# Kernel tuning notes

Hardware: AMD Instinct MI355X
Metric: run time of the kernel (lower is better)

The kernel has to match this reference:

```python
import jax, jax.numpy as jnp
import numpy as np

B, S, M = 1, 1024, 1024          # batch, seq, hidden
H, D, KV = 16, 64, 8             # q heads, head dim, kv heads (kv hardcoded=8)
G = H // KV                      # gqa groups
FF = 3072                        # expert/shared mlp inner dim (hardcoded)
E, K = 64, 8                     # experts, topk (hardcoded)
CAP = 2 * K * S * B // E         # static expert capacity (>= dynamic max -> no drops)
RMS_EPS = 1e-6
F32_EPS = 1.1920929e-07          # torch.finfo(float32).eps


def _rms(x, w, eps=RMS_EPS):
    v = jnp.mean(x * x, axis=-1, keepdims=True)
    return w * (x * jax.lax.rsqrt(v + eps))


def _rotate_half(x):
    d = x.shape[-1] // 2
    return jnp.concatenate([-x[..., d:], x[..., :d]], axis=-1)


def _mlp(x, gu_w, dn_w):
    gu = x @ gu_w                       # [..., 2*FF]
    x1, x2 = gu[..., :FF], gu[..., FF:]
    return (x1 * jax.nn.silu(x2)) @ dn_w


def _topkgating(logits):
    # logits: [T, E] fp32
    gates = jax.nn.softmax(logits, axis=1)
    topv, topi = jax.lax.top_k(gates, K)                 # [T, K]
    gates_s = jnp.clip(jnp.sum(topv, axis=1, keepdims=True), F32_EPS)
    router_probs = gates / gates_s                        # [T, E]
    # priority: cumsum of one-hot over flattened (K, T) order, matching torch
    idx_flat = topi.T.reshape(-1)                         # [K*T]
    mask = jax.nn.one_hot(idx_flat, E, dtype=jnp.int32)   # [K*T, E]
    prio = jnp.cumsum(mask, axis=0) * mask - 1            # [K*T, E]
    prio = prio.reshape(K, -1, E).transpose(1, 0, 2).max(axis=1)  # [T, E]
    valid = (prio >= 0) & (prio < CAP)
    prio = jnp.where(valid, prio, 0)
    dispatch = jax.nn.one_hot(prio, CAP, dtype=jnp.float32) * valid[..., None]  # [T,E,C]
    combine = router_probs[..., None] * dispatch                                 # [T,E,C]
    return combine, dispatch


def setup_inputs() -> dict:
    key = jax.random.key(0)
    ks = jax.random.split(key, 10)
    sc = 0.02
    inv_freq = 1.0 / (10000.0 ** (jnp.arange(0, D, 2, dtype=jnp.float32) / D))
    t = jnp.arange(S, dtype=jnp.float32)
    freqs = jnp.outer(t, inv_freq)                        # [S, D/2]
    emb = jnp.concatenate([freqs, freqs], axis=-1)        # [S, D]
    cos = jnp.broadcast_to(jnp.cos(emb), (B, S, D))
    sin = jnp.broadcast_to(jnp.sin(emb), (B, S, D))
    return {
        'hidden_states': jax.random.normal(ks[0], (B, S, M), jnp.float32),
        'cos': cos,
        'sin': sin,
        'ln1_w': jnp.ones((M,), jnp.float32),
        'ln2_w': jnp.ones((M,), jnp.float32),
        'qkv_w': jax.random.normal(ks[1], (M, (H + 2 * KV) * D), jnp.float32) * sc,
        'o_w': jax.random.normal(ks[2], (H * D, M), jnp.float32) * sc,
        'qn_w': jnp.ones((D,), jnp.float32),
        'kn_w': jnp.ones((D,), jnp.float32),
        'shared_gu_w': jax.random.normal(ks[3], (M, 2 * FF), jnp.float32) * sc,
        'shared_dn_w': jax.random.normal(ks[4], (FF, M), jnp.float32) * sc,
        'gate_w': jax.random.normal(ks[5], (M, E), jnp.float32) * sc,
        'expert_gu_w': jax.random.normal(ks[6], (E, M, 2 * FF), jnp.float32) * sc,
        'expert_dn_w': jax.random.normal(ks[7], (E, FF, M), jnp.float32) * sc,
    }


def reference(hidden_states, cos, sin, ln1_w, ln2_w, qkv_w, o_w, qn_w, kn_w,
              shared_gu_w, shared_dn_w, gate_w, expert_gu_w, expert_dn_w):
    # ---- attention block ----
    hn = _rms(hidden_states, ln1_w)                       # input layernorm
    qkv = (hn @ qkv_w).reshape(B, S, KV, G + 2, D)
    q = qkv[..., :G, :].reshape(B, S, H, D).transpose(0, 2, 1, 3)   # [B,H,S,D]
    k = qkv[..., G, :].transpose(0, 2, 1, 3)                        # [B,KV,S,D]
    v = qkv[..., G + 1, :].transpose(0, 2, 1, 3)                    # [B,KV,S,D]
    c, s_ = cos[:, None], sin[:, None]                    # [B,1,S,D]
    q = q * c + _rotate_half(q) * s_
    k = k * c + _rotate_half(k) * s_
    q = _rms(q, qn_w)
    k = _rms(k, kn_w)
    k = jnp.repeat(k, G, axis=1)                          # GQA expand -> [B,H,S,D]
    v = jnp.repeat(v, G, axis=1)
    scores = jnp.einsum('bhqd,bhkd->bhqk', q, k) / np.sqrt(D)
    causal = jnp.tril(jnp.ones((S, S), bool))
    scores = jnp.where(causal, scores, -1e9)
    attn = jax.nn.softmax(scores, axis=-1)
    ao = jnp.einsum('bhqk,bhkd->bhqd', attn, v).transpose(0, 2, 1, 3).reshape(B, S, H * D)
    h = hidden_states + ao @ o_w                          # residual

    # ---- MoE block ----
    h2 = _rms(h, ln2_w)                                   # post-attn layernorm
    shared = _mlp(h2, shared_gu_w, shared_dn_w)           # [B,S,M]
    x = h2.reshape(-1, M)                                 # [T,M]
    logits = x @ gate_w                                   # fp32 gate
    combine, dispatch = _topkgating(logits)               # [T,E,C]
    dispatched = jnp.einsum('sec,sm->ecm', dispatch, x)   # [E,C,M]
    gu = jnp.einsum('ecm,emf->ecf', dispatched, expert_gu_w)  # [E,C,2*FF]
    x1, x2 = gu[..., :FF], gu[..., FF:]
    eo = jnp.einsum('ecf,efm->ecm', x1 * jax.nn.silu(x2), expert_dn_w)  # [E,C,M]
    combined = jnp.einsum('sec,ecm->sm', combine, eo).reshape(B, S, M)
    return h + shared + combined
```

## Files before the change

kernel.cpp:

```cpp
#include <hip/hip_runtime.h>

#define S 1024
#define MDIM 1024
#define NH 16
#define HD 64
#define NKV 8
#define FF 3072
#define NE 64
#define TOPK 8
#define CAP 256

typedef unsigned short u16;
typedef __attribute__((ext_vector_type(8))) short bf16x8;
typedef __attribute__((ext_vector_type(4))) float f32x4;

__device__ __forceinline__ u16 f2bf(float f) {
    union { float f; unsigned u; } x; x.f = f;
    unsigned r = x.u + 0x7FFFu + ((x.u >> 16) & 1u);
    return (u16)(r >> 16);
}
__device__ __forceinline__ float bf2f(u16 b) {
    union { unsigned u; float f; } x; x.u = ((unsigned)b) << 16;
    return x.f;
}
__device__ __forceinline__ void split1(float x, u16& h, u16& l) {
    h = f2bf(x);
    l = f2bf(x - bf2f(h));
}
__device__ __forceinline__ int swzcol(int row, int G) { return 8 * (G ^ ((row >> 3) & 3)); }

__device__ __forceinline__ void gl_lds16(const u16* g, u16* l) {
    __builtin_amdgcn_global_load_lds(
        (const __attribute__((address_space(1))) unsigned int*)g,
        (__attribute__((address_space(3))) unsigned int*)l, 16, 0, 0);
}

__global__ __launch_bounds__(256) void k_rms1(const float* __restrict__ x,
                                              const float* __restrict__ w,
                                              u16* __restrict__ ohi,
                                              u16* __restrict__ olo) {
    int s = blockIdx.x;
    const float* row = x + (size_t)s * MDIM;
    float v[4]; float ss = 0.f;
#pragma unroll
    for (int i = 0; i < 4; ++i) { v[i] = row[threadIdx.x + i * 256]; ss += v[i] * v[i]; }
#pragma unroll
    for (int of = 32; of; of >>= 1) ss += __shfl_xor(ss, of);
    __shared__ float red[4];
    int wid = threadIdx.x >> 6;
    if ((threadIdx.x & 63) == 0) red[wid] = ss;
    __syncthreads();
    float tot = red[0] + red[1] + red[2] + red[3];
    float sc = rsqrtf(tot * (1.f / MDIM) + 1e-6f);
#pragma unroll
    for (int i = 0; i < 4; ++i) {
        int c = threadIdx.x + i * 256;
        float ov = v[i] * sc * w[c];
        u16 hh, ll; split1(ov, hh, ll);
        ohi[(size_t)s * MDIM + c] = hh;
        olo[(size_t)s * MDIM + c] = ll;
    }
}

template <int EPI>
__global__ __launch_bounds__(256) void k_gemm_split(
    const u16* __restrict__ Ahi, const u16* __restrict__ Alo, int lda,
    const float* __restrict__ B, int ldb,
    float* __restrict__ C, int ldc,
    const float* __restrict__ resid, int M, int K) {
    int m0 = blockIdx.y * 64;
    int n0 = blockIdx.x * 64;
    __shared__ u16 Ah[2][64][32];
    __shared__ u16 Al[2][64][32];
    __shared__ u16 Bh[2][64][40];
    __shared__ u16 Bl[2][64][40];
    int tid = threadIdx.x, lane = tid & 63, wid = tid >> 6;
    int wm = (wid >> 1) * 32, wn = (wid & 1) * 32;
    f32x4 acc[2][2] = {};

    int rt = wid * 16 + (lane >> 2);
    int gsrc = (lane & 3) ^ ((lane >> 4) & 3);
    const u16* ahb = Ahi + (size_t)(m0 + rt) * lda + gsrc * 8;
    const u16* alb = Alo + (size_t)(m0 + rt) * lda + gsrc * 8;

    int nB = tid & 63, kbB = tid >> 6;
    int colB = swzcol(nB, kbB);
    float rb[8];
    auto loadB = [&](int k0) {
        const float* bp = B + (size_t)(k0 + kbB * 8) * ldb + n0 + nB;
#pragma unroll
        for (int i = 0; i < 8; ++i) rb[i] = bp[(size_t)i * ldb];
    };
    auto stageA = [&](int b, int k0) {
        gl_lds16(ahb + k0, &Ah[b][wid * 16][0]);
        gl_lds16(alb + k0, &Al[b][wid * 16][0]);
    };
    auto writeB = [&](int b) {
        bf16x8 hh, ll;
#pragma unroll
        for (int i = 0; i < 8; ++i) { u16 h, l; split1(rb[i], h, l); hh[i] = (short)h; ll[i] = (short)l; }
        *(bf16x8*)&Bh[b][nB][colB] = hh;
        *(bf16x8*)&Bl[b][nB][colB] = ll;
    };

    loadB(0); stageA(0, 0); writeB(0);
    __syncthreads();
    int NT = K / 32;
    for (int t = 0; t < NT; ++t) {
        int c = t & 1;
        if (t + 1 < NT) { loadB((t + 1) * 32); stageA(1 - c, (t + 1) * 32); }
        bf16x8 ah[2], al[2], bh[2], bl[2];
#pragma unroll
        for (int mi = 0; mi < 2; ++mi) {
            int r = wm + mi * 16 + (lane & 15);
            int cA = 8 * ((lane >> 4) ^ ((r >> 2) & 3));
            ah[mi] = *(const bf16x8*)&Ah[c][r][cA];
            al[mi] = *(const bf16x8*)&Al[c][r][cA];
        }
#pragma unroll
        for (int ni = 0; ni < 2; ++ni) {
            int r = wn + ni * 16 + (lane & 15);
            int cc = swzcol(r, lane >> 4);
            bh[ni] = *(const bf16x8*)&Bh[c][r][cc];
            bl[ni] = *(const bf16x8*)&Bl[c][r][cc];
        }
#pragma unroll
        for (int mi = 0; mi < 2; ++mi)
#pragma unroll
            for (int ni = 0; ni < 2; ++ni) {
                acc[mi][ni] = __builtin_amdgcn_mfma_f32_16x16x32_bf16(ah[mi], bh[ni], acc[mi][ni], 0, 0, 0);
                acc[mi][ni] = __builtin_amdgcn_mfma_f32_16x16x32_bf16(ah[mi], bl[ni], acc[mi][ni], 0, 0, 0);
                acc[mi][ni] = __builtin_amdgcn_mfma_f32_16x16x32_bf16(al[mi], bh[ni], acc[mi][ni], 0, 0, 0);
            }
        if (t + 1 < NT) { writeB(1 - c); __syncthreads(); }
    }
#pragma unroll
    for (int mi = 0; mi < 2; ++mi)
#pragma unroll
        for (int ni = 0; ni < 2; ++ni)
#pragma unroll
            for (int r = 0; r < 4; ++r) {
                int row = m0 + wm + mi * 16 + (lane >> 4) * 4 + r;
                int col = n0 + wn + ni * 16 + (lane & 15);
                float v = acc[mi][ni][r];
                if constexpr (EPI == 1) v += resid[(size_t)row * ldc + col];
                C[(size_t)row * ldc + col] = v;
            }
}

template <int TM, int TN, bool SWIGLU>
__global__ __launch_bounds__(256) void k_gemm_bf(
    const u16* __restrict__ A, int lda, long sAe,
    const float* __restrict__ B, long sBe, int ldb,
    u16* __restrict__ C, int ldc, long sCe,
    int K, int pairOff,
    const int* __restrict__ counts, const int* __restrict__ rowidx,
    const u16* __restrict__ Ash, const float* __restrict__ Bsh,
    u16* __restrict__ Csh, int Msh) {
    int z = blockIdx.z;
    int tid = threadIdx.x, lane = tid & 63, wid = tid >> 6;
    int M, m0;
    const int* ridx = nullptr;
    if (z >= NE) {
        int mslot = (z - NE) * 2 + blockIdx.y;
        m0 = mslot * TM;
        M = Msh;
        A = Ash; B = Bsh; C = Csh;
        if (m0 >= M) return;
    } else {
        M = counts[z];
        m0 = blockIdx.y * TM;
        if (m0 >= M) return;
        A += (size_t)z * sAe;
        B += (size_t)z * sBe;
        C += (size_t)z * sCe;
        if (rowidx) ridx = rowidx + z * CAP;
    }
    int n0 = blockIdx.x * TN;

    __shared__ u16 As[2][TM][32];
    __shared__ u16 Bs[2][TN][40];
    __shared__ u16 B2s[2][SWIGLU ? TN : 1][40];

    constexpr int MF = TM / 32;
    constexpr int NI = TN / 32;
    int wm = (wid >> 1) * (TM / 2), wn = (wid & 1) * (TN / 2);

    f32x4 acc[MF][NI] = {};
    f32x4 acc2[SWIGLU ? MF : 1][NI] = {};

    constexpr int NCH = TM / 16;
    constexpr int CPW = (NCH + 3) / 4;
    int arow_in = lane >> 2;
    int gsrc = (lane & 3) ^ ((lane >> 4) & 3);
    const u16* abase[CPW];
#pragma unroll
    for (int i = 0; i < CPW; ++i) {
        int ch = wid + i * 4;
        const u16* p = A;
        if (ch < NCH) {
            int rti = ch * 16 + arow_in;
            int gm = m0 + rti;
            long grow = (gm < M) ? (ridx ? (long)ridx[gm] : (long)gm) : 0;
            p = A + grow * (size_t)lda + gsrc * 8;
        }
        abase[i] = p;
    }
    auto stageA = [&](int b, int k0) {
#pragma unroll
        for (int i = 0; i < CPW; ++i) {
            int ch = wid + i * 4;
            if (ch < NCH) gl_lds16(abase[i] + k0, &As[b][ch * 16][0]);
        }
    };

    constexpr int NKG = 256 / TN;
    constexpr int OPT = 4 / NKG;
    int nB = tid % TN, kgB = tid / TN;
    float rb[OPT][8], rg[SWIGLU ? OPT : 1][8];
    auto loadB = [&](int k0) {
        const float* bp = B + (size_t)(k0 + kgB * OPT * 8) * ldb + n0 + nB;
#pragma unroll
        for (int j = 0; j < OPT; ++j)
#pragma unroll
            for (int i = 0; i < 8; ++i) {
                rb[j][i] = bp[(size_t)(j * 8 + i) * ldb];
                if constexpr (SWIGLU) rg[j][i] = bp[(size_t)(j * 8 + i) * ldb + pairOff];
            }
    };
    auto writeB = [&](int b) {
#pragma unroll
        for (int j = 0; j < OPT; ++j) {
            int col = swzcol(nB, kgB * OPT + j);
            bf16x8 v;
#pragma unroll
            for (int i = 0; i < 8; ++i) v[i] = (short)f2bf(rb[j][i]);
            *(bf16x8*)&Bs[b][nB][col] = v;
            if constexpr (SWIGLU) {
                bf16x8 g;
#pragma unroll
                for (int i = 0; i < 8; ++i) g[i] = (short)f2bf(rg[j][i]);
                *(bf16x8*)&B2s[b][nB][col] = g;
            }
        }
    };

    loadB(0); stageA(0, 0); writeB(0);
    __syncthreads();
    int NT = K / 32;
    for (int t = 0; t < NT; ++t) {
        int c = t & 1;
        if (t + 1 < NT) { loadB((t + 1) * 32); stageA(1 - c, (t + 1) * 32); }
        bf16x8 af[MF], bfr[NI], gfr[SWIGLU ? NI : 1];
#pragma unroll
        for (int mi = 0; mi < MF; ++mi) {
            int r = wm + mi * 16 + (lane & 15);
            int cA = 8 * ((lane >> 4) ^ ((r >> 2) & 3));
            af[mi] = *(const bf16x8*)&As[c][r][cA];
        }
#pragma unroll
        for (int ni = 0; ni < NI; ++ni) {
            int r = wn + ni * 16 + (lane & 15);
            int cB = swzcol(r, lane >> 4);
            bfr[ni] = *(const bf16x8*)&Bs[c][r][cB];
            if constexpr (SWIGLU) gfr[ni] = *(const bf16x8*)&B2s[c][r][cB];
        }
#pragma unroll
        for (int mi = 0; mi < MF; ++mi)
#pragma unroll
            for (int ni = 0; ni < NI; ++ni) {
                acc[mi][ni] = __builtin_amdgcn_mfma_f32_16x16x32_bf16(af[mi], bfr[ni], acc[mi][ni], 0, 0, 0);
                if constexpr (SWIGLU)
                    acc2[mi][ni] = __builtin_amdgcn_mfma_f32_16x16x32_bf16(af[mi], gfr[ni], acc2[mi][ni], 0, 0, 0);
            }
        if (t + 1 < NT) { writeB(1 - c); __syncthreads(); }
    }
#pragma unroll
    for (int mi = 0; mi < MF; ++mi)
#pragma unroll
        for (int ni = 0; ni < NI; ++ni)
#pragma unroll
            for (int r = 0; r < 4; ++r) {
                int row = m0 + wm + mi * 16 + (lane >> 4) * 4 + r;
                int col = n0 + wn + ni * 16 + (lane & 15);
                if (row >= M) continue;
                float x1 = acc[mi][ni][r];
                if constexpr (SWIGLU) {
                    float x2 = acc2[mi][ni][r];
                    x1 = x1 * (x2 / (1.f + __expf(-x2)));
                }
                C[(size_t)row * ldc + col] = f2bf(x1);
            }
}

__global__ __launch_bounds__(256) void k_rope(const float* __restrict__ qkv,
                                              const float* __restrict__ cosb,
                                              const float* __restrict__ sinb,
                                              const float* __restrict__ qn_w,
                                              const float* __restrict__ kn_w,
                                              u16* __restrict__ qh, u16* __restrict__ ql,
                                              u16* __restrict__ kh, u16* __restrict__ kl,
                                              u16* __restrict__ vh, u16* __restrict__ vl) {
    int wid = threadIdx.x >> 6, lane = threadIdx.x & 63;
    int idx = blockIdx.x * 4 + wid;
    int s = idx >> 3, j = idx & 7;
    const float* base = qkv + (size_t)s * 2048 + j * 256;
    float c = cosb[s * HD + lane], sn = sinb[s * HD + lane];
    u16 hh, ll;
    split1(base[192 + lane], hh, ll);
    vh[((size_t)j * S + s) * HD + lane] = hh;
    vl[((size_t)j * S + s) * HD + lane] = ll;
#pragma unroll
    for (int r = 0; r < 3; ++r) {
        float x = base[r * 64 + lane];
        float xp = __shfl_xor(x, 32);
        float rot = (lane < 32) ? -xp : xp;
        float y = x * c + rot * sn;
        float ss = y * y;
#pragma unroll
        for (int o = 32; o; o >>= 1) ss += __shfl_xor(ss, o);
        float scale = rsqrtf(ss * (1.f / 64.f) + 1e-6f);
        float outv = y * scale * ((r == 2) ? kn_w[lane] : qn_w[lane]);
        split1(outv, hh, ll);
        if (r == 2) {
            kh[((size_t)j * S + s) * HD + lane] = hh;
            kl[((size_t)j * S + s) * HD + lane] = ll;
        } else {
            qh[((size_t)(j * 2 + r) * S + s) * HD + lane] = hh;
            ql[((size_t)(j * 2 + r) * S + s) * HD + lane] = ll;
        }
    }
}

__global__ __launch_bounds__(256) void k_scores(const u16* __restrict__ qh, const u16* __restrict__ ql,
                                                const u16* __restrict__ kmh, const u16* __restrict__ kml,
                                                float* __restrict__ scores) {
    int kt = blockIdx.x, qt = blockIdx.y, h = blockIdx.z;
    if (kt > qt) return;
    size_t qoff = (size_t)h * S * HD;
    size_t koff = (size_t)(h >> 1) * S * HD;
    int lane = threadIdx.x & 63, wid = threadIdx.x >> 6;
    int wq = (wid >> 1) * 32, wk = (wid & 1) * 32;
    int q0 = qt * 64, k0 = kt * 64;
    f32x4 acc[2][2] = {};
#pragma unroll
    for (int ks = 0; ks < 2; ++ks) {
        bf16x8 ah[2], al[2], bh[2], bl[2];
#pragma unroll
        for (int mi = 0; mi < 2; ++mi) {
            size_t o = qoff + (size_t)(q0 + wq + mi * 16 + (lane & 15)) * HD + ks * 32 + (lane >> 4) * 8;
            ah[mi] = *(const bf16x8*)(qh + o);
            al[mi] = *(const bf16x8*)(ql + o);
        }
#pragma unroll
        for (int ni = 0; ni < 2; ++ni) {
            size_t o = koff + (size_t)(k0 + wk + ni * 16 + (lane & 15)) * HD + ks * 32 + (lane >> 4) * 8;
            bh[ni] = *(const bf16x8*)(kmh + o);
            bl[ni] = *(const bf16x8*)(kml + o);
        }
#pragma unroll
        for (int mi = 0; mi < 2; ++mi)
#pragma unroll
            for (int ni = 0; ni < 2; ++ni) {
                acc[mi][ni] = __builtin_amdgcn_mfma_f32_16x16x32_bf16(ah[mi], bh[ni], acc[mi][ni], 0, 0, 0);
                acc[mi][ni] = __builtin_amdgcn_mfma_f32_16x16x32_bf16(ah[mi], bl[ni], acc[mi][ni], 0, 0, 0);
                acc[mi][ni] = __builtin_amdgcn_mfma_f32_16x16x32_bf16(al[mi], bh[ni], acc[mi][ni], 0, 0, 0);
            }
    }
#pragma unroll
    for (int mi = 0; mi < 2; ++mi)
#pragma unroll
        for (int ni = 0; ni < 2; ++ni)
#pragma unroll
            for (int r = 0; r < 4; ++r) {
                int row = q0 + wq + mi * 16 + (lane >> 4) * 4 + r;
                int col = k0 + wk + ni * 16 + (lane & 15);
                scores[(size_t)h * S * S + (size_t)row * S + col] = acc[mi][ni][r] * 0.125f;
            }
}

__global__ __launch_bounds__(256) void k_softmax(const float* __restrict__ scores,
                                                 u16* __restrict__ Ph, u16* __restrict__ Pl) {
    int wid = threadIdx.x >> 6, lane = threadIdx.x & 63;
    int q = blockIdx.x * 4 + wid, h = blockIdx.y;
    const float* row = scores + (size_t)h * S * S + (size_t)q * S;
    size_t po = (size_t)h * S * S + (size_t)q * S;
    int L = q + 1;
    int wlim = ((q >> 6) + 1) * 64;
    float v[16];
    float mx = -1e30f;
#pragma unroll
    for (int i = 0; i < 16; ++i) {
        int idx = lane + i * 64;
        v[i] = (idx < L) ? row[idx] : -1e30f;
        mx = fmaxf(mx, v[i]);
    }
#pragma unroll
    for (int o = 32; o; o >>= 1) mx = fmaxf(mx, __shfl_xor(mx, o));
    float sum = 0.f;
#pragma unroll
    for (int i = 0; i < 16; ++i) {
        int idx = lane + i * 64;
        v[i] = (idx < L) ? __expf(v[i] - mx) : 0.f;
        sum += v[i];
    }
#pragma unroll
    for (int o = 32; o; o >>= 1) sum += __shfl_xor(sum, o);
    float inv = 1.f / sum;
#pragma unroll
    for (int i = 0; i < 16; ++i) {
        int idx = lane + i * 64;
        if (idx < wlim) {
            u16 hh, ll;
            split1(v[i] * inv, hh, ll);
            Ph[po + idx] = hh;
            Pl[po + idx] = ll;
        }
    }
}

__global__ __launch_bounds__(256) void k_pv(const u16* __restrict__ Ph, const u16* __restrict__ Pl,
                                            const u16* __restrict__ vmh, const u16* __restrict__ vml,
                                            u16* __restrict__ aoh, u16* __restrict__ aol) {
    int qt = blockIdx.x, h = blockIdx.y;
    size_t poff = (size_t)h * S * S;
    size_t voff = (size_t)(h >> 1) * S * HD;
    __shared__ u16 Vh[64][72];
    __shared__ u16 Vl[64][72];
    int tid = threadIdx.x, lane = tid & 63, wid = tid >> 6;
    int wq = (wid >> 1) * 32, wd = (wid & 1) * 32;
    int q0 = qt * 64;
    f32x4 acc[2][2] = {};
    int kmax = (qt + 1) * 64;
    for (int kc = 0; kc < kmax; kc += 64) {
#pragma unroll
        for (int i = 0; i < 16; ++i) {
            int idx = tid + i * 256;
            int kr = idx >> 6, d = idx & 63;
            Vh[d][kr] = vmh[voff + (size_t)(kc + kr) * HD + d];
            Vl[d][kr] = vml[voff + (size_t)(kc + kr) * HD + d];
        }
        __syncthreads();
#pragma unroll
        for (int ks = 0; ks < 2; ++ks) {
            bf16x8 ph[2], pl[2], vh[2], vl[2];
#pragma unroll
            for (int mi = 0; mi < 2; ++mi) {
                size_t o = poff + (size_t)(q0 + wq + mi * 16 + (lane & 15)) * S + kc + ks * 32 + (lane >> 4) * 8;
                ph[mi] = *(const bf16x8*)(Ph + o);
                pl[mi] = *(const bf16x8*)(Pl + o);
            }
#pragma unroll
            for (int ni = 0; ni < 2; ++ni) {
                vh[ni] = *(const bf16x8*)&Vh[wd + ni * 16 + (lane & 15)][ks * 32 + (lane >> 4) * 8];
                vl[ni] = *(const bf16x8*)&Vl[wd + ni * 16 + (lane & 15)][ks * 32 + (lane >> 4) * 8];
            }
#pragma unroll
            for (int mi = 0; mi < 2; ++mi)
#pragma unroll
                for (int ni = 0; ni < 2; ++ni) {
                    acc[mi][ni] = __builtin_amdgcn_mfma_f32_16x16x32_bf16(ph[mi], vh[ni], acc[mi][ni], 0, 0, 0);
                    acc[mi][ni] = __builtin_amdgcn_mfma_f32_16x16x32_bf16(ph[mi], vl[ni], acc[mi][ni], 0, 0, 0);
                    acc[mi][ni] = __builtin_amdgcn_mfma_f32_16x16x32_bf16(pl[mi], vh[ni], acc[mi][ni], 0, 0, 0);
                }
        }
        __syncthreads();
    }
#pragma unroll
    for (int mi = 0; mi < 2; ++mi)
#pragma unroll
        for (int ni = 0; ni < 2; ++ni)
#pragma unroll
            for (int r = 0; r < 4; ++r) {
                int row = q0 + wq + mi * 16 + (lane >> 4) * 4 + r;
                int col = wd + ni * 16 + (lane & 15);
                u16 hh, ll; split1(acc[mi][ni][r], hh, ll);
                aoh[(size_t)row * MDIM + h * HD + col] = hh;
                aol[(size_t)row * MDIM + h * HD + col] = ll;
            }
}

__global__ __launch_bounds__(256) void k_rms2_router(const float* __restrict__ h,
                                                     const float* __restrict__ w,
                                                     const float* __restrict__ gw,
                                                     u16* __restrict__ h2b,
                                                     int* __restrict__ topi,
                                                     float* __restrict__ wts) {
    __shared__ float xr[1024];
    __shared__ float part[4][64];
    __shared__ float red[4];
    int s = blockIdx.x, tid = threadIdx.x;
    const float* row = h + (size_t)s * MDIM;
    float v[4]; float ss = 0.f;
#pragma unroll
    for (int i = 0; i < 4; ++i) { v[i] = row[tid + i * 256]; ss += v[i] * v[i]; }
#pragma unroll
    for (int of = 32; of; of >>= 1) ss += __shfl_xor(ss, of);
    if ((tid & 63) == 0) red[tid >> 6] = ss;
    __syncthreads();
    float tot = red[0] + red[1] + red[2] + red[3];
    float sc = rsqrtf(tot * (1.f / MDIM) + 1e-6f);
#pragma unroll
    for (int i = 0; i < 4; ++i) {
        int c = tid + i * 256;
        float ov = v[i] * sc * w[c];
        xr[c] = ov;
        h2b[(size_t)s * MDIM + c] = f2bf(ov);
    }
    __syncthreads();
    int e = tid & 63, qq = tid >> 6;
    float acc = 0.f;
    for (int i = 0; i < 256; ++i) acc += xr[qq * 256 + i] * gw[(size_t)(qq * 256 + i) * NE + e];
    part[qq][e] = acc;
    __syncthreads();
    if (tid < 64) {
        int lane = tid;
        float lg = part[0][lane] + part[1][lane] + part[2][lane] + part[3][lane];
        float mx = lg;
#pragma unroll
        for (int o = 32; o; o >>= 1) mx = fmaxf(mx, __shfl_xor(mx, o));
        float ex = __expf(lg - mx);
        float sum = ex;
#pragma unroll
        for (int o = 32; o; o >>= 1) sum += __shfl_xor(sum, o);
        float g = ex / sum;
        float cur = g;
        float tv[TOPK]; int ti[TOPK];
        float tsum = 0.f;
#pragma unroll
        for (int k = 0; k < TOPK; ++k) {
            float vv = cur; int ii = lane;
#pragma unroll
            for (int o = 32; o; o >>= 1) {
                float vo = __shfl_xor(vv, o);
                int io = __shfl_xor(ii, o);
                if (vo > vv || (vo == vv && io < ii)) { vv = vo; ii = io; }
            }
            tv[k] = vv; ti[k] = ii; tsum += vv;
            if (lane == ii) cur = -1.f;
        }
        float gs = fmaxf(tsum, 1.1920929e-07f);
        if (lane == 0) {
#pragma unroll
            for (int k = 0; k < TOPK; ++k) {
                topi[s * TOPK + k] = ti[k];
                wts[s * TOPK + k] = tv[k] / gs;
            }
        }
    }
}

__global__ __launch_bounds__(512) void k_slots(const int* __restrict__ topi, int* __restrict__ slots,
                                               int* __restrict__ counts, int* __restrict__ etok) {
    __shared__ int tl[S * TOPK];
    __shared__ int cnt[TOPK][NE];
    __shared__ int base[TOPK][NE];
    int tid = threadIdx.x;
    for (int i = tid; i < S * TOPK; i += 512) tl[i] = topi[i];
    ((int*)cnt)[tid] = 0;
    __syncthreads();
    for (int i = tid; i < S * TOPK; i += 512)
        atomicAdd(&cnt[i & 7][tl[i]], 1);
    __syncthreads();
    if (tid < NE) {
        int acc = 0;
#pragma unroll
        for (int k = 0; k < TOPK; ++k) { base[k][tid] = acc; acc += cnt[k][tid]; }
        counts[tid] = acc < CAP ? acc : CAP;
    }
    __syncthreads();
    int k = tid >> 6, e = tid & 63;
    int rank = base[k][e];
    for (int s = 0; s < S; ++s) {
        if (tl[s * TOPK + k] == e) {
            if (rank < CAP) { slots[s * TOPK + k] = rank; etok[e * CAP + rank] = s; }
            else slots[s * TOPK + k] = -1;
            rank++;
        }
    }
}

__global__ __launch_bounds__(256) void k_combine(const float* __restrict__ h,
                                                 const u16* __restrict__ sh,
                                                 const u16* __restrict__ eo,
                                                 const int* __restrict__ topi,
                                                 const int* __restrict__ slots,
                                                 const float* __restrict__ wts,
                                                 float* __restrict__ out) {
    int s = blockIdx.x, t = threadIdx.x;
    float w[TOPK]; int off[TOPK];
#pragma unroll
    for (int k = 0; k < TOPK; ++k) {
        int sl = slots[s * TOPK + k];
        int ee = topi[s * TOPK + k];
        w[k] = wts[s * TOPK + k];
        off[k] = (sl >= 0) ? ee * CAP + sl : -1;
    }
#pragma unroll
    for (int i = 0; i < 4; ++i) {
        int col = t + i * 256;
        float acc = h[(size_t)s * MDIM + col] + bf2f(sh[(size_t)s * MDIM + col]);
#pragma unroll
        for (int k = 0; k < TOPK; ++k)
            if (off[k] >= 0) acc += w[k] * bf2f(eo[(size_t)off[k] * MDIM + col]);
        out[(size_t)s * MDIM + col] = acc;
    }
}

extern "C" void kernel_launch(void* const* d_in, const int* in_sizes, int n_in,
                              void* d_out, int out_size, void* d_ws, size_t ws_size,
                              hipStream_t stream) {
    (void)in_sizes; (void)n_in; (void)out_size; (void)ws_size;
    const float* hidden = (const float*)d_in[0];
    const float* cosb   = (const float*)d_in[1];
    const float* sinb   = (const float*)d_in[2];
    const float* ln1_w  = (const float*)d_in[3];
    const float* ln2_w  = (const float*)d_in[4];
    const float* qkv_w  = (const float*)d_in[5];
    const float* o_w    = (const float*)d_in[6];
    const float* qn_w   = (const float*)d_in[7];
    const float* kn_w   = (const float*)d_in[8];
    const float* sgu_w  = (const float*)d_in[9];
    const float* sdn_w  = (const float*)d_in[10];
    const float* gate_w = (const float*)d_in[11];
    const float* egu_w  = (const float*)d_in[12];
    const float* edn_w  = (const float*)d_in[13];
    float* out = (float*)d_out;

    char* ws = (char*)d_ws;
    size_t off = 0;
    auto alloc = [&](size_t bytes) -> void* {
        void* p = ws + off;
        off = (off + bytes + 255) & ~(size_t)255;
        return p;
    };
    u16*   hn_hi   = (u16*)  alloc((size_t)S * MDIM * 2);
    u16*   hn_lo   = (u16*)  alloc((size_t)S * MDIM * 2);
    float* qkvb    = (float*)alloc((size_t)S * 2048 * 4);
    u16*   qhb     = (u16*)  alloc((size_t)NH * S * HD * 2);
    u16*   qlb     = (u16*)  alloc((size_t)NH * S * HD * 2);
    u16*   khb     = (u16*)  alloc((size_t)NKV * S * HD * 2);
    u16*   klb     = (u16*)  alloc((size_t)NKV * S * HD * 2);
    u16*   vhb     = (u16*)  alloc((size_t)NKV * S * HD * 2);
    u16*   vlb     = (u16*)  alloc((size_t)NKV * S * HD * 2);
    float* scores  = (float*)alloc((size_t)NH * S * S * 4);
    u16*   Phb     = (u16*)  alloc((size_t)NH * S * S * 2);
    u16*   Plb     = (u16*)  alloc((size_t)NH * S * S * 2);
    u16*   ao_hi   = (u16*)  alloc((size_t)S * MDIM * 2);
    u16*   ao_lo   = (u16*)  alloc((size_t)S * MDIM * 2);
    float* hbuf    = (float*)alloc((size_t)S * MDIM * 4);
    u16*   h2b     = (u16*)  alloc((size_t)S * MDIM * 2);
    u16*   gatedS  = (u16*)  alloc((size_t)S * FF * 2);
    u16*   sharedO = (u16*)  alloc((size_t)S * MDIM * 2);
    int*   topi    = (int*)  alloc((size_t)S * TOPK * 4);
    float* wts     = (float*)alloc((size_t)S * TOPK * 4);
    int*   slots   = (int*)  alloc((size_t)S * TOPK * 4);
    int*   counts  = (int*)  alloc((size_t)NE * 4);
    int*   etok    = (int*)  alloc((size_t)NE * CAP * 4);
    u16*   egated  = (u16*)  alloc((size_t)NE * CAP * FF * 2);
    u16*   eo      = (u16*)  alloc((size_t)NE * CAP * MDIM * 2);

    k_rms1<<<dim3(S), 256, 0, stream>>>(hidden, ln1_w, hn_hi, hn_lo);
    k_gemm_split<0><<<dim3(2048 / 64, S / 64), 256, 0, stream>>>(
        hn_hi, hn_lo, MDIM, qkv_w, 2048, qkvb, 2048, nullptr, S, MDIM);
    k_rope<<<dim3(S * NKV / 4), 256, 0, stream>>>(qkvb, cosb, sinb, qn_w, kn_w,
                                                  qhb, qlb, khb, klb, vhb, vlb);
    k_scores<<<dim3(16, 16, NH), 256, 0, stream>>>(qhb, qlb, khb, klb, scores);
    k_softmax<<<dim3(S / 4, NH), 256, 0, stream>>>(scores, Phb, Plb);
    k_pv<<<dim3(16, NH), 256, 0, stream>>>(Phb, Plb, vhb, vlb, ao_hi, ao_lo);
    k_gemm_split<1><<<dim3(MDIM / 64, S / 64), 256, 0, stream>>>(
        ao_hi, ao_lo, MDIM, o_w, MDIM, hbuf, MDIM, hidden, S, MDIM);
    k_rms2_router<<<dim3(S), 256, 0, stream>>>(hbuf, ln2_w, gate_w, h2b, topi, wts);
    k_slots<<<dim3(1), 512, 0, stream>>>(topi, slots, counts, etok);
    k_gemm_bf<160, 64, true><<<dim3(FF / 64, 2, NE + 4), 256, 0, stream>>>(
        h2b, MDIM, 0, egu_w, (long)MDIM * 2 * FF, 2 * FF,
        egated, FF, (long)CAP * FF, MDIM, FF, counts, etok,
        h2b, sgu_w, gatedS, S);
    k_gemm_bf<160, 128, false><<<dim3(MDIM / 128, 2, NE + 4), 256, 0, stream>>>(
        egated, FF, (long)CAP * FF, edn_w, (long)FF * MDIM, MDIM,
        eo, MDIM, (long)CAP * MDIM, FF, 0, counts, nullptr,
        gatedS, sdn_w, sharedO, S);
    k_combine<<<dim3(S), 256, 0, stream>>>(hbuf, sharedO, eo, topi, slots, wts, out);
}
```

Before: 1.033 ms.

## Fuse attention into flash-style kernel and remap down-proj grid for XCD locality

```diff
diff --git a/kernel.cpp b/kernel.cpp
--- a/kernel.cpp
+++ b/kernel.cpp
@@ -148,7 +148,7 @@
             }
 }
 
-template <int TM, int TN, bool SWIGLU>
+template <int TM, int TN, bool SWIGLU, bool XCD1D>
 __global__ __launch_bounds__(256) void k_gemm_bf(
     const u16* __restrict__ A, int lda, long sAe,
     const float* __restrict__ B, long sBe, int ldb,
@@ -157,26 +157,33 @@
     const int* __restrict__ counts, const int* __restrict__ rowidx,
     const u16* __restrict__ Ash, const float* __restrict__ Bsh,
     u16* __restrict__ Csh, int Msh) {
-    int z = blockIdx.z;
+    int z, byy, bxx;
+    if constexpr (XCD1D) {
+        int id = blockIdx.x;
+        if (id < 1024) { byy = id >> 9; int t = id & 511; z = ((t >> 6) << 3) | (t & 7); bxx = (t >> 3) & 7; }
+        else { int ms = id - 1024; z = NE + (ms >> 4); byy = (ms >> 3) & 1; bxx = ms & 7; }
+    } else {
+        z = blockIdx.z; byy = blockIdx.y; bxx = blockIdx.x;
+    }
     int tid = threadIdx.x, lane = tid & 63, wid = tid >> 6;
     int M, m0;
     const int* ridx = nullptr;
     if (z >= NE) {
-        int mslot = (z - NE) * 2 + blockIdx.y;
+        int mslot = (z - NE) * 2 + byy;
         m0 = mslot * TM;
         M = Msh;
         A = Ash; B = Bsh; C = Csh;
         if (m0 >= M) return;
     } else {
         M = counts[z];
-        m0 = blockIdx.y * TM;
+        m0 = byy * TM;
         if (m0 >= M) return;
         A += (size_t)z * sAe;
         B += (size_t)z * sBe;
         C += (size_t)z * sCe;
         if (rowidx) ridx = rowidx + z * CAP;
     }
-    int n0 = blockIdx.x * TN;
+    int n0 = bxx * TN;
 
     __shared__ u16 As[2][TM][32];
     __shared__ u16 Bs[2][TN][40];
@@ -332,107 +339,41 @@
     }
 }
 
-__global__ __launch_bounds__(256) void k_scores(const u16* __restrict__ qh, const u16* __restrict__ ql,
-                                                const u16* __restrict__ kmh, const u16* __restrict__ kml,
-                                                float* __restrict__ scores) {
-    int kt = blockIdx.x, qt = blockIdx.y, h = blockIdx.z;
-    if (kt > qt) return;
+__global__ __launch_bounds__(256) void k_attn(const u16* __restrict__ qh, const u16* __restrict__ ql,
+                                              const u16* __restrict__ kmh, const u16* __restrict__ kml,
+                                              const u16* __restrict__ vmh, const u16* __restrict__ vml,
+                                              u16* __restrict__ aoh, u16* __restrict__ aol) {
+    int qt = 15 - blockIdx.x;
+    int h = blockIdx.y;
+    int q0 = qt * 64;
     size_t qoff = (size_t)h * S * HD;
     size_t koff = (size_t)(h >> 1) * S * HD;
-    int lane = threadIdx.x & 63, wid = threadIdx.x >> 6;
-    int wq = (wid >> 1) * 32, wk = (wid & 1) * 32;
-    int q0 = qt * 64, k0 = kt * 64;
-    f32x4 acc[2][2] = {};
-#pragma unroll
-    for (int ks = 0; ks < 2; ++ks) {
-        bf16x8 ah[2], al[2], bh[2], bl[2];
-#pragma unroll
-        for (int mi = 0; mi < 2; ++mi) {
-            size_t o = qoff + (size_t)(q0 + wq + mi * 16 + (lane & 15)) * HD + ks * 32 + (lane >> 4) * 8;
-            ah[mi] = *(const bf16x8*)(qh + o);
-            al[mi] = *(const bf16x8*)(ql + o);
-        }
-#pragma unroll
-        for (int ni = 0; ni < 2; ++ni) {
-            size_t o = koff + (size_t)(k0 + wk + ni * 16 + (lane & 15)) * HD + ks * 32 + (lane >> 4) * 8;
-            bh[ni] = *(const bf16x8*)(kmh + o);
-            bl[ni] = *(const bf16x8*)(kml + o);
-        }
-#pragma unroll
-        for (int mi = 0; mi < 2; ++mi)
-#pragma unroll
-            for (int ni = 0; ni < 2; ++ni) {
-                acc[mi][ni] = __builtin_amdgcn_mfma_f32_16x16x32_bf16(ah[mi], bh[ni], acc[mi][ni], 0, 0, 0);
-                acc[mi][ni] = __builtin_amdgcn_mfma_f32_16x16x32_bf16(ah[mi], bl[ni], acc[mi][ni], 0, 0, 0);
-                acc[mi][ni] = __builtin_amdgcn_mfma_f32_16x16x32_bf16(al[mi], bh[ni], acc[mi][ni], 0, 0, 0);
-            }
-    }
-#pragma unroll
-    for (int mi = 0; mi < 2; ++mi)
-#pragma unroll
-        for (int ni = 0; ni < 2; ++ni)
-#pragma unroll
-            for (int r = 0; r < 4; ++r) {
-                int row = q0 + wq + mi * 16 + (lane >> 4) * 4 + r;
-                int col = k0 + wk + ni * 16 + (lane & 15);
-                scores[(size_t)h * S * S + (size_t)row * S + col] = acc[mi][ni][r] * 0.125f;
-            }
-}
-
-__global__ __launch_bounds__(256) void k_softmax(const float* __restrict__ scores,
-                                                 u16* __restrict__ Ph, u16* __restrict__ Pl) {
-    int wid = threadIdx.x >> 6, lane = threadIdx.x & 63;
-    int q = blockIdx.x * 4 + wid, h = blockIdx.y;
-    const float* row = scores + (size_t)h * S * S + (size_t)q * S;
-    size_t po = (size_t)h * S * S + (size_t)q * S;
-    int L = q + 1;
-    int wlim = ((q >> 6) + 1) * 64;
-    float v[16];
-    float mx = -1e30f;
-#pragma unroll
-    for (int i = 0; i < 16; ++i) {
-        int idx = lane + i * 64;
-        v[i] = (idx < L) ? row[idx] : -1e30f;
-        mx = fmaxf(mx, v[i]);
-    }
-#pragma unroll
-    for (int o = 32; o; o >>= 1) mx = fmaxf(mx, __shfl_xor(mx, o));
-    float sum = 0.f;
-#pragma unroll
-    for (int i = 0; i < 16; ++i) {
-        int idx = lane + i * 64;
-        v[i] = (idx < L) ? __expf(v[i] - mx) : 0.f;
-        sum += v[i];
-    }
-#pragma unroll
-    for (int o = 32; o; o >>= 1) sum += __shfl_xor(sum, o);
-    float inv = 1.f / sum;
-#pragma unroll
-    for (int i = 0; i < 16; ++i) {
-        int idx = lane + i * 64;
-        if (idx < wlim) {
-            u16 hh, ll;
-            split1(v[i] * inv, hh, ll);
-            Ph[po + idx] = hh;
-            Pl[po + idx] = ll;
-        }
-    }
-}
-
-__global__ __launch_bounds__(256) void k_pv(const u16* __restrict__ Ph, const u16* __restrict__ Pl,
-                                            const u16* __restrict__ vmh, const u16* __restrict__ vml,
-                                            u16* __restrict__ aoh, u16* __restrict__ aol) {
-    int qt = blockIdx.x, h = blockIdx.y;
-    size_t poff = (size_t)h * S * S;
-    size_t voff = (size_t)(h >> 1) * S * HD;
+    size_t voff = koff;
+
     __shared__ u16 Vh[64][72];
     __shared__ u16 Vl[64][72];
-    int tid = threadIdx.x, lane = tid & 63, wid = tid >> 6;
-    int wq = (wid >> 1) * 32, wd = (wid & 1) * 32;
-    int q0 = qt * 64;
-    f32x4 acc[2][2] = {};
-    int kmax = (qt + 1) * 64;
-    for (int kc = 0; kc < kmax; kc += 64) {
+    __shared__ u16 Ph_l[4][16][72];
+    __shared__ u16 Pl_l[4][16][72];
+
+    int tid = threadIdx.x, lane = tid & 63, w = tid >> 6;
+    int rgrp = lane >> 4;
+    int l16 = lane & 15;
+
+    bf16x8 qfh[2], qfl[2];
+#pragma unroll
+    for (int ks = 0; ks < 2; ++ks) {
+        size_t o = qoff + (size_t)(q0 + w * 16 + l16) * HD + ks * 32 + rgrp * 8;
+        qfh[ks] = *(const bf16x8*)(qh + o);
+        qfl[ks] = *(const bf16x8*)(ql + o);
+    }
+
+    float m_[4], l_[4];
+    f32x4 o_[4] = {};
+#pragma unroll
+    for (int r = 0; r < 4; ++r) { m_[r] = -1e30f; l_[r] = 0.f; }
+
+    for (int kt = 0; kt <= qt; ++kt) {
+        int kc = kt * 64;
 #pragma unroll
         for (int i = 0; i < 16; ++i) {
             int idx = tid + i * 256;
@@ -441,43 +382,98 @@
             Vl[d][kr] = vml[voff + (size_t)(kc + kr) * HD + d];
         }
         __syncthreads();
+
+        f32x4 sacc[4] = {};
 #pragma unroll
         for (int ks = 0; ks < 2; ++ks) {
-            bf16x8 ph[2], pl[2], vh[2], vl[2];
-#pragma unroll
-            for (int mi = 0; mi < 2; ++mi) {
-                size_t o = poff + (size_t)(q0 + wq + mi * 16 + (lane & 15)) * S + kc + ks * 32 + (lane >> 4) * 8;
-                ph[mi] = *(const bf16x8*)(Ph + o);
-                pl[mi] = *(const bf16x8*)(Pl + o);
-            }
-#pragma unroll
-            for (int ni = 0; ni < 2; ++ni) {
-                vh[ni] = *(const bf16x8*)&Vh[wd + ni * 16 + (lane & 15)][ks * 32 + (lane >> 4) * 8];
-                vl[ni] = *(const bf16x8*)&Vl[wd + ni * 16 + (lane & 15)][ks * 32 + (lane >> 4) * 8];
-            }
-#pragma unroll
-            for (int mi = 0; mi < 2; ++mi)
-#pragma unroll
-                for (int ni = 0; ni < 2; ++ni) {
-                    acc[mi][ni] = __builtin_amdgcn_mfma_f32_16x16x32_bf16(ph[mi], vh[ni], acc[mi][ni], 0, 0, 0);
-                    acc[mi][ni] = __builtin_amdgcn_mfma_f32_16x16x32_bf16(ph[mi], vl[ni], acc[mi][ni], 0, 0, 0);
-                    acc[mi][ni] = __builtin_amdgcn_mfma_f32_16x16x32_bf16(pl[mi], vh[ni], acc[mi][ni], 0, 0, 0);
-                }
+            bf16x8 bh[4], bl[4];
+#pragma unroll
+            for (int ni = 0; ni < 4; ++ni) {
+                size_t o = koff + (size_t)(kc + ni * 16 + l16) * HD + ks * 32 + rgrp * 8;
+                bh[ni] = *(const bf16x8*)(kmh + o);
+                bl[ni] = *(const bf16x8*)(kml + o);
+            }
+#pragma unroll
+            for (int ni = 0; ni < 4; ++ni) {
+                sacc[ni] = __builtin_amdgcn_mfma_f32_16x16x32_bf16(qfh[ks], bh[ni], sacc[ni], 0, 0, 0);
+                sacc[ni] = __builtin_amdgcn_mfma_f32_16x16x32_bf16(qfh[ks], bl[ni], sacc[ni], 0, 0, 0);
+                sacc[ni] = __builtin_amdgcn_mfma_f32_16x16x32_bf16(qfl[ks], bh[ni], sacc[ni], 0, 0, 0);
+            }
+        }
+#pragma unroll
+        for (int ni = 0; ni < 4; ++ni)
+#pragma unroll
+            for (int r = 0; r < 4; ++r) {
+                int qrow = q0 + w * 16 + rgrp * 4 + r;
+                int col = kc + ni * 16 + l16;
+                float sv = sacc[ni][r] * 0.125f;
+                sacc[ni][r] = (col > qrow) ? -1e30f : sv;
+            }
+        float pm[4], mnew[4], sf[4], ps[4];
+#pragma unroll
+        for (int r = 0; r < 4; ++r) {
+            float mx = fmaxf(fmaxf(sacc[0][r], sacc[1][r]), fmaxf(sacc[2][r], sacc[3][r]));
+#pragma unroll
+            for (int off = 1; off < 16; off <<= 1) mx = fmaxf(mx, __shfl_xor(mx, off));
+            pm[r] = mx;
+            mnew[r] = fmaxf(m_[r], pm[r]);
+            sf[r] = __expf(m_[r] - mnew[r]);
+            m_[r] = mnew[r];
+            ps[r] = 0.f;
+        }
+#pragma unroll
+        for (int ni = 0; ni < 4; ++ni)
+#pragma unroll
+            for (int r = 0; r < 4; ++r) {
+                float p = __expf(sacc[ni][r] - mnew[r]);
+                ps[r] += p;
+                u16 hh, ll; split1(p, hh, ll);
+                Ph_l[w][rgrp * 4 + r][ni * 16 + l16] = hh;
+                Pl_l[w][rgrp * 4 + r][ni * 16 + l16] = ll;
+            }
+#pragma unroll
+        for (int r = 0; r < 4; ++r) {
+            float s_ = ps[r];
+#pragma unroll
+            for (int off = 1; off < 16; off <<= 1) s_ += __shfl_xor(s_, off);
+            l_[r] = l_[r] * sf[r] + s_;
+        }
+#pragma unroll
+        for (int ni = 0; ni < 4; ++ni)
+#pragma unroll
+            for (int r = 0; r < 4; ++r) o_[ni][r] *= sf[r];
+#pragma unroll
+        for (int ks2 = 0; ks2 < 2; ++ks2) {
+            bf16x8 pah = *(const bf16x8*)&Ph_l[w][l16][ks2 * 32 + rgrp * 8];
+            bf16x8 pal = *(const bf16x8*)&Pl_l[w][l16][ks2 * 32 + rgrp * 8];
+            bf16x8 vbh[4], vbl[4];
+#pragma unroll
+            for (int ni = 0; ni < 4; ++ni) {
+                vbh[ni] = *(const bf16x8*)&Vh[ni * 16 + l16][ks2 * 32 + rgrp * 8];
+                vbl[ni] = *(const bf16x8*)&Vl[ni * 16 + l16][ks2 * 32 + rgrp * 8];
+            }
+#pragma unroll
+            for (int ni = 0; ni < 4; ++ni) {
+                o_[ni] = __builtin_amdgcn_mfma_f32_16x16x32_bf16(pah, vbh[ni], o_[ni], 0, 0, 0);
+                o_[ni] = __builtin_amdgcn_mfma_f32_16x16x32_bf16(pah, vbl[ni], o_[ni], 0, 0, 0);
+                o_[ni] = __builtin_amdgcn_mfma_f32_16x16x32_bf16(pal, vbh[ni], o_[ni], 0, 0, 0);
+            }
         }
         __syncthreads();
     }
 #pragma unroll
-    for (int mi = 0; mi < 2; ++mi)
-#pragma unroll
-        for (int ni = 0; ni < 2; ++ni)
-#pragma unroll
-            for (int r = 0; r < 4; ++r) {
-                int row = q0 + wq + mi * 16 + (lane >> 4) * 4 + r;
-                int col = wd + ni * 16 + (lane & 15);
-                u16 hh, ll; split1(acc[mi][ni][r], hh, ll);
-                aoh[(size_t)row * MDIM + h * HD + col] = hh;
-                aol[(size_t)row * MDIM + h * HD + col] = ll;
-            }
+    for (int r = 0; r < 4; ++r) {
+        float inv = 1.f / l_[r];
+        int row = q0 + w * 16 + rgrp * 4 + r;
+#pragma unroll
+        for (int ni = 0; ni < 4; ++ni) {
+            float val = o_[ni][r] * inv;
+            u16 hh, ll; split1(val, hh, ll);
+            size_t o = (size_t)row * MDIM + h * HD + ni * 16 + l16;
+            aoh[o] = hh;
+            aol[o] = ll;
+        }
+    }
 }
 
 __global__ __launch_bounds__(256) void k_rms2_router(const float* __restrict__ h,
@@ -643,9 +639,6 @@
     u16*   klb     = (u16*)  alloc((size_t)NKV * S * HD * 2);
     u16*   vhb     = (u16*)  alloc((size_t)NKV * S * HD * 2);
     u16*   vlb     = (u16*)  alloc((size_t)NKV * S * HD * 2);
-    float* scores  = (float*)alloc((size_t)NH * S * S * 4);
-    u16*   Phb     = (u16*)  alloc((size_t)NH * S * S * 2);
-    u16*   Plb     = (u16*)  alloc((size_t)NH * S * S * 2);
     u16*   ao_hi   = (u16*)  alloc((size_t)S * MDIM * 2);
     u16*   ao_lo   = (u16*)  alloc((size_t)S * MDIM * 2);
     float* hbuf    = (float*)alloc((size_t)S * MDIM * 4);
@@ -665,18 +658,16 @@
         hn_hi, hn_lo, MDIM, qkv_w, 2048, qkvb, 2048, nullptr, S, MDIM);
     k_rope<<<dim3(S * NKV / 4), 256, 0, stream>>>(qkvb, cosb, sinb, qn_w, kn_w,
                                                   qhb, qlb, khb, klb, vhb, vlb);
-    k_scores<<<dim3(16, 16, NH), 256, 0, stream>>>(qhb, qlb, khb, klb, scores);
-    k_softmax<<<dim3(S / 4, NH), 256, 0, stream>>>(scores, Phb, Plb);
-    k_pv<<<dim3(16, NH), 256, 0, stream>>>(Phb, Plb, vhb, vlb, ao_hi, ao_lo);
+    k_attn<<<dim3(16, NH), 256, 0, stream>>>(qhb, qlb, khb, klb, vhb, vlb, ao_hi, ao_lo);
     k_gemm_split<1><<<dim3(MDIM / 64, S / 64), 256, 0, stream>>>(
         ao_hi, ao_lo, MDIM, o_w, MDIM, hbuf, MDIM, hidden, S, MDIM);
     k_rms2_router<<<dim3(S), 256, 0, stream>>>(hbuf, ln2_w, gate_w, h2b, topi, wts);
     k_slots<<<dim3(1), 512, 0, stream>>>(topi, slots, counts, etok);
-    k_gemm_bf<160, 64, true><<<dim3(FF / 64, 2, NE + 4), 256, 0, stream>>>(
+    k_gemm_bf<160, 64, true, false><<<dim3(FF / 64, 2, NE + 4), 256, 0, stream>>>(
         h2b, MDIM, 0, egu_w, (long)MDIM * 2 * FF, 2 * FF,
         egated, FF, (long)CAP * FF, MDIM, FF, counts, etok,
         h2b, sgu_w, gatedS, S);
-    k_gemm_bf<160, 128, false><<<dim3(MDIM / 128, 2, NE + 4), 256, 0, stream>>>(
+    k_gemm_bf<160, 128, false, true><<<dim3(1088, 1, 1), 256, 0, stream>>>(
         egated, FF, (long)CAP * FF, edn_w, (long)FF * MDIM, MDIM,
         eo, MDIM, (long)CAP * MDIM, FF, 0, counts, nullptr,
         gatedS, sdn_w, sharedO, S);
```

New measurement: 902.7 us, median of 3. 12.6% less time.
